# Optimization experiments

Measured on AMD Instinct MI355X. Metric: run time of the kernel, lower is better.

The kernel has to match this reference:

```python
import jax, jax.numpy as jnp
import numpy as np

B, L, H, S2V = 32, 1024, 256, 256
STEP = 1          # HP_SLSTM_step window size
EPS = 1e-3        # LayerNorm eps (added to std, torch-style unbiased std)
NUM_LAYERS = 4
# LayerNorm param row indices in ln_a/ln_b:
# 0..5 -> word gates f1,f2,f3,f4,i,o ; 6 gd ; 7 go ; 8 gf ; 9 gi ; 10 gg


def _ln(x, a, b):
    # torch LayerNorm variant: unbiased std, eps added to std (not var)
    mean = x.mean(-1, keepdims=True)
    d = x - mean
    std = jnp.sqrt((d * d).sum(-1, keepdims=True) / (x.shape[-1] - 1))
    return a * d / (std + EPS) + b


def setup_inputs() -> dict:
    key = jax.random.key(0)
    ks = jax.random.split(key, 16)
    p = lambda k, shp: 0.1 * jax.random.normal(k, shp, dtype=jnp.float32)
    return {
        "word_inputs": jax.random.normal(ks[0], (B, L, H), dtype=jnp.float32),
        "sent_embeddings": jax.random.normal(ks[1], (B, S2V), dtype=jnp.float32),
        "mask": jnp.ones((B, L), dtype=jnp.float32),
        "h0": jax.random.uniform(ks[2], (B, L, H), minval=-0.05, maxval=0.05, dtype=jnp.float32),
        "c0": jax.random.uniform(ks[3], (B, L, H), minval=-0.05, maxval=0.05, dtype=jnp.float32),
        "Wx_g": p(ks[4], (6, H, H)),
        "Wh_g": p(ks[5], (6, 2 * H, H)),
        "Wi_g": p(ks[6], (6, H, H)),
        "Wd_g": p(ks[7], (6, H, H)),
        "b_g": p(ks[8], (6, H)),
        "gWx": p(ks[9], (4, H, H)),   # dummy gates d,i,o,f
        "gWh": p(ks[10], (4, H, H)),
        "gWg": p(ks[11], (4, S2V, H)),  # d,i,o,g
        "gb": p(ks[12], (4, H)),
        "ln_a": jnp.ones((11, H), dtype=jnp.float32),
        "ln_b": jnp.zeros((11, H), dtype=jnp.float32),
        "num_layers": NUM_LAYERS,
    }


def _win_sums(t):
    # sum of left-shifted (before) and right-shifted (after) neighbor states
    bef = jnp.zeros_like(t)
    aft = jnp.zeros_like(t)
    for s in range(1, STEP + 1):
        bef = bef + jnp.pad(t[:, :-s], ((0, 0), (s, 0), (0, 0)))
        aft = aft + jnp.pad(t[:, s:], ((0, 0), (0, s), (0, 0)))
    return bef.reshape(-1, t.shape[-1]), aft.reshape(-1, t.shape[-1])


def reference(word_inputs, sent_embeddings, mask, h0, c0, Wx_g, Wh_g, Wi_g,
              Wd_g, b_g, gWx, gWh, gWg, gb, ln_a, ln_b, num_layers):
    Bs, Ls, Hs = word_inputs.shape
    seq_mask = mask[..., None]                      # (B,L,1)
    msm = (mask * 1e25 - 1e25)[..., None]           # softmax mask (B,L,1)
    emb_h = (word_inputs * seq_mask).reshape(-1, Hs)  # fixed word embedding states
    emb_c = emb_h
    h = h0 * seq_mask
    c = c0 * seq_mask
    dh = h.mean(axis=1)                             # dummy (sentence) node (B,H)
    dc = c.mean(axis=1)

    for _ in range(num_layers):
        comb = h.mean(axis=1)                       # (B,H)
        rh = h.reshape(-1, Hs)                      # (B*L,H)
        tdh = (dh[:, None, :] * seq_mask).reshape(-1, Hs)
        tdc = (dc[:, None, :] * seq_mask).reshape(-1, Hs)

        # --- dummy (sentence-level) node gates ---
        gd = jax.nn.sigmoid(_ln(dh @ gWx[0] + sent_embeddings @ gWg[0] + comb @ gWh[0] + gb[0], ln_a[6], ln_b[6]))
        gi = jax.nn.sigmoid(_ln(dh @ gWx[1] + sent_embeddings @ gWg[1] + comb @ gWh[1], ln_a[9], ln_b[9]) + gb[1])  # bias outside LN, as in source
        gg = sent_embeddings @ gWg[3]
        go = jax.nn.sigmoid(_ln(dh @ gWx[2] + sent_embeddings @ gWg[2] + comb @ gWh[2] + gb[2], ln_a[7], ln_b[7]))
        gf = jax.nn.sigmoid(_ln(tdh @ gWx[3] + rh @ gWh[3] + gb[3], ln_a[8], ln_b[8]))
        gf = gf.reshape(Bs, Ls, Hs) + msm
        scores = jax.nn.softmax(jnp.concatenate([gf, gd[:, None, :], gi[:, None, :]], axis=1), axis=1)
        f_w = scores[:, :Ls]
        d_w = scores[:, Ls]
        i_w = scores[:, Ls + 1]
        dc_new = jnp.sum(f_w * c, axis=1) + d_w * dc + i_w * jnp.tanh(_ln(gg, ln_a[10], ln_b[10]))
        dh_new = go * jnp.tanh(dc_new)

        # --- word node gates (windowed message passing) ---
        hb, ha = _win_sums(h)
        cb, ca = _win_sums(c)
        cat_h = jnp.concatenate([hb, ha], axis=1)   # (B*L, 2H)
        pre = (jnp.einsum('nh,ghk->gnk', emb_h, Wx_g)
               + jnp.einsum('nc,gck->gnk', cat_h, Wh_g)
               + jnp.einsum('nh,ghk->gnk', rh, Wi_g)
               + jnp.einsum('nh,ghk->gnk', tdh, Wd_g)
               + b_g[:, None, :])                   # (6, B*L, H)
        gates = jax.nn.sigmoid(_ln(pre, ln_a[:6, None, :], ln_b[:6, None, :]))
        five = jax.nn.softmax(gates[:5], axis=0)    # normalize f1..f4,i
        f1, f2, f3, f4, i_t = five
        o_t = gates[5]
        c_new = cb * f1 + ca * f2 + emb_c * f3 + tdc * f4 + c.reshape(-1, Hs) * i_t
        h_new = o_t * jnp.tanh(c_new)
        h = h_new.reshape(Bs, Ls, Hs) * seq_mask
        c = c_new.reshape(Bs, Ls, Hs) * seq_mask
        dh, dc = dh_new, dc_new
    return h
```

## Files before the change

kernel.cpp:

```cpp
#include <hip/hip_runtime.h>
#include <cstddef>

#define Bz 32
#define Lz 1024
#define Hz 256
#define Nz (Bz*Lz)
#define NHz ((size_t)Nz*Hz)
#define BHz (Bz*Hz)
#define EPSz 1e-3f
#define NLAYERS 4
#define NCH 64
#define NTC 112
#define CHR 16384

typedef __bf16 bf8_t __attribute__((ext_vector_type(8)));
typedef __bf16 bf4_t __attribute__((ext_vector_type(4)));
typedef float  f4_t  __attribute__((ext_vector_type(4)));

__device__ inline float sigmoidf(float x){ return 1.f/(1.f+expf(-x)); }
__device__ inline float fsig(float x){ return __builtin_amdgcn_rcpf(1.f + __expf(-x)); }
__device__ inline float ftanh(float x){ return 1.f - 2.f*__builtin_amdgcn_rcpf(__expf(2.f*x)+1.f); }

__device__ inline void gl_lds16(const void* g, void* l){
  __builtin_amdgcn_global_load_lds(
      (const __attribute__((address_space(1))) void*)g,
      (__attribute__((address_space(3))) void*)l, 16, 0, 0);
}

__device__ inline float2 block_sum2(float a, float b, float* red){
  #pragma unroll
  for (int off=32; off; off>>=1){ a += __shfl_down(a,off,64); b += __shfl_down(b,off,64); }
  int w = threadIdx.x>>6;
  __syncthreads();
  if ((threadIdx.x&63)==0){ red[w]=a; red[4+w]=b; }
  __syncthreads();
  return make_float2(red[0]+red[1]+red[2]+red[3], red[4]+red[5]+red[6]+red[7]);
}

__device__ inline float ln_block(float v, const float* la, const float* lb, int t, float* red){
  float2 ss = block_sum2(v, v*v, red);
  float mean = ss.x*(1.f/Hz);
  float var  = (ss.y - (float)Hz*mean*mean)*(1.f/(Hz-1));
  float isd  = 1.f/(sqrtf(fmaxf(var,0.f))+EPSz);
  return la[t]*(v-mean)*isd + lb[t];
}

__global__ void k_initb(const float* __restrict__ word, const float* __restrict__ h0,
                        const float* __restrict__ c0, const float* __restrict__ mask,
                        __bf16* __restrict__ xe, __bf16* __restrict__ h, __bf16* __restrict__ c){
  int tid = blockIdx.x*256 + threadIdx.x;
  int n = tid >> 5; int c8 = (tid & 31)*8;
  float m = mask[n];
  size_t off = (size_t)n*Hz + c8;
  const float4* wv = (const float4*)(word + off);
  float4 w0 = wv[0], w1 = wv[1];
  bf8_t o;
  o[0]=(__bf16)(w0.x*m); o[1]=(__bf16)(w0.y*m); o[2]=(__bf16)(w0.z*m); o[3]=(__bf16)(w0.w*m);
  o[4]=(__bf16)(w1.x*m); o[5]=(__bf16)(w1.y*m); o[6]=(__bf16)(w1.z*m); o[7]=(__bf16)(w1.w*m);
  *(bf8_t*)(xe + off) = o;
  const float4* hv = (const float4*)(h0 + off);
  float4 a0 = hv[0], a1 = hv[1];
  o[0]=(__bf16)(a0.x*m); o[1]=(__bf16)(a0.y*m); o[2]=(__bf16)(a0.z*m); o[3]=(__bf16)(a0.w*m);
  o[4]=(__bf16)(a1.x*m); o[5]=(__bf16)(a1.y*m); o[6]=(__bf16)(a1.z*m); o[7]=(__bf16)(a1.w*m);
  *(bf8_t*)(h + off) = o;
  const float4* cv = (const float4*)(c0 + off);
  float4 b0 = cv[0], b1 = cv[1];
  o[0]=(__bf16)(b0.x*m); o[1]=(__bf16)(b0.y*m); o[2]=(__bf16)(b0.z*m); o[3]=(__bf16)(b0.w*m);
  o[4]=(__bf16)(b1.x*m); o[5]=(__bf16)(b1.y*m); o[6]=(__bf16)(b1.z*m); o[7]=(__bf16)(b1.w*m);
  *(bf8_t*)(c + off) = o;
}

__global__ void k_packWt(const float* __restrict__ Wx, const float* __restrict__ Wh,
                         const float* __restrict__ Wi, const float* __restrict__ gWh3,
                         __bf16* __restrict__ Wt, __bf16* __restrict__ zbuf){
  int tid = blockIdx.x*256 + threadIdx.x;
  if (tid < 128) zbuf[tid] = (__bf16)0.f;
  int col = tid >> 7;
  int k0  = (tid & 127) << 3;
  if (col >= 1792) return;
  int g = col >> 8, cg = col & 255;
  int seg = k0 >> 8, kl0 = k0 & 255;
  bf8_t o;
  #pragma unroll
  for (int j=0;j<8;j++){
    int kl = kl0 + j;
    float v = 0.f;
    if (g < 6){
      if (seg==0)      v = Wx[((size_t)g*256 + kl)*256 + cg];
      else if (seg==1) v = Wh[((size_t)g*512 + kl)*256 + cg];
      else if (seg==2) v = Wh[((size_t)g*512 + 256 + kl)*256 + cg];
      else             v = Wi[((size_t)g*256 + kl)*256 + cg];
    } else {
      if (seg==3)      v = gWh3[(size_t)kl*256 + cg];
    }
    o[j] = (__bf16)v;
  }
  *(bf8_t*)(Wt + (size_t)col*1024 + k0) = o;
}

__global__ void k_meanpb(const __bf16* __restrict__ x, float* __restrict__ part){
  int b = blockIdx.x, ch = blockIdx.y, t = threadIdx.x;
  const __bf16* p = x + ((size_t)b*Lz + ch*128)*Hz + t;
  float s = 0.f;
  #pragma unroll 4
  for (int l=0;l<128;l++) s += (float)p[(size_t)l*Hz];
  part[(b*8+ch)*Hz + t] = s;
}
__global__ void k_comb8(const float* __restrict__ part, float* __restrict__ o){
  int b = blockIdx.x, t = threadIdx.x;
  float s = 0.f;
  #pragma unroll
  for (int ch=0;ch<8;ch++) s += part[(b*8+ch)*Hz + t];
  o[b*Hz+t] = s*(1.f/Lz);
}

__global__ __launch_bounds__(256) void k_small(
    const float* __restrict__ dh, const float* __restrict__ comb, const float* __restrict__ sent,
    const float* __restrict__ gWx, const float* __restrict__ gWh, const float* __restrict__ gWg,
    const float* __restrict__ gb, const float* __restrict__ Wd_g,
    const float* __restrict__ ln_a, const float* __restrict__ ln_b,
    float* __restrict__ gd, float* __restrict__ gi, float* __restrict__ go,
    float* __restrict__ tgg, float* __restrict__ dhWd7){
  int b = blockIdx.x, which = blockIdx.y, t = threadIdx.x;
  __shared__ float sdh[Hz], sse[Hz], sco[Hz];
  __shared__ float red[8];
  sdh[t]=dh[b*Hz+t]; sse[t]=sent[b*Hz+t]; sco[t]=comb[b*Hz+t];
  __syncthreads();
  float acc=0.f;
  if (which < 3){
    const float* W0 = gWx + which*Hz*Hz;
    const float* W1 = gWg + which*Hz*Hz;
    const float* W2 = gWh + which*Hz*Hz;
    for (int k=0;k<Hz;k++) acc += sdh[k]*W0[k*Hz+t] + sse[k]*W1[k*Hz+t] + sco[k]*W2[k*Hz+t];
    if (which==0){
      float r = ln_block(acc + gb[0*Hz+t], ln_a+6*Hz, ln_b+6*Hz, t, red);
      gd[b*Hz+t] = sigmoidf(r);
    } else if (which==1){
      float r = ln_block(acc, ln_a+9*Hz, ln_b+9*Hz, t, red);
      gi[b*Hz+t] = sigmoidf(r + gb[1*Hz+t]);
    } else {
      float r = ln_block(acc + gb[2*Hz+t], ln_a+7*Hz, ln_b+7*Hz, t, red);
      go[b*Hz+t] = sigmoidf(r);
    }
  } else if (which == 3){
    const float* W = gWg + 3*Hz*Hz;
    for (int k=0;k<Hz;k++) acc += sse[k]*W[k*Hz+t];
    float r = ln_block(acc, ln_a+10*Hz, ln_b+10*Hz, t, red);
    tgg[b*Hz+t] = tanhf(r);
  } else if (which == 4){
    const float* W = gWx + 3*Hz*Hz;
    for (int k=0;k<Hz;k++) acc += sdh[k]*W[k*Hz+t];
    dhWd7[(6*Bz + b)*Hz + t] = acc;
  } else {
    int g = which-5;
    const float* W = Wd_g + g*Hz*Hz;
    for (int k=0;k<Hz;k++) acc += sdh[k]*W[k*Hz+t];
    dhWd7[(g*Bz + b)*Hz + t] = acc;
  }
}

__global__ __launch_bounds__(256) void k_gemm(
    const __bf16* __restrict__ xe, const __bf16* __restrict__ h,
    const __bf16* __restrict__ Wt, const __bf16* __restrict__ zbuf,
    __bf16* __restrict__ pre, int n_base){
  __shared__ __align__(16) __bf16 sA[128*64];
  __shared__ __align__(16) __bf16 sB[128*64];
  int t = threadIdx.x;
  int w = t>>6, lane = t&63;
  int m16 = lane&15, p = lane>>4;
  int bx = blockIdx.x, by = blockIdx.y;
  int row0 = n_base + bx*128;
  int coltile = by*128;

  f4_t acc[4][4];
  #pragma unroll
  for (int i=0;i<4;i++)
    #pragma unroll
    for (int j=0;j<4;j++) acc[i][j] = (f4_t){0.f,0.f,0.f,0.f};

  int srr = t>>3;
  int sck = t&7;
  int arow = (w&1)*64 + m16;
  int brow = (w>>1)*64 + m16;
  int swz  = m16 & 7;

  const char* Ab = (const char*)sA;
  const char* Bb = (const char*)sB;

  int seg_s = (by >= 12) ? 3 : 0;
  #pragma unroll 1
  for (int seg=seg_s; seg<4; ++seg){
    #pragma unroll 1
    for (int ks=0; ks<4; ++ks){
      __syncthreads();
      int kloc = ks*64;
      #pragma unroll
      for (int it=0; it<4; ++it){
        int drow = it*32 + srr;
        int sc = (sck ^ (drow&7)) << 3;
        int r = row0 + drow;
        const __bf16* asrc;
        if (seg==0)      asrc = xe + (size_t)r*Hz + kloc + sc;
        else if (seg==3) asrc = h + (size_t)r*Hz + kloc + sc;
        else if (seg==1) asrc = ((r&1023)==0)    ? zbuf : h + ((size_t)(r-1)*Hz + kloc + sc);
        else             asrc = ((r&1023)==1023) ? zbuf : h + ((size_t)(r+1)*Hz + kloc + sc);
        gl_lds16(asrc, sA + drow*64 + sck*8);
        const __bf16* bsrc = Wt + (size_t)(coltile + drow)*1024 + seg*256 + kloc + sc;
        gl_lds16(bsrc, sB + drow*64 + sck*8);
      }
      __syncthreads();
      #pragma unroll
      for (int kb=0; kb<2; ++kb){
        bf8_t a[4], bb[4];
        int cofs = ((kb*4 + p) ^ swz) << 4;
        #pragma unroll
        for (int tr=0;tr<4;tr++)
          a[tr] = *(const bf8_t*)(Ab + (arow + tr*16)*128 + cofs);
        #pragma unroll
        for (int tc=0;tc<4;tc++)
          bb[tc] = *(const bf8_t*)(Bb + (brow + tc*16)*128 + cofs);
        #pragma unroll
        for (int tr=0;tr<4;tr++)
          #pragma unroll
          for (int tc=0;tc<4;tc++)
            acc[tr][tc] = __builtin_amdgcn_mfma_f32_16x16x32_bf16(a[tr], bb[tc], acc[tr][tc], 0, 0, 0);
      }
    }
  }

  int trg0 = (bx*128 + (w&1)*64) >> 4;
  int tcg0 = (coltile + (w>>1)*64) >> 4;
  #pragma unroll
  for (int tr=0;tr<4;tr++){
    #pragma unroll
    for (int tc=0;tc<4;tc++){
      size_t tile = (size_t)(trg0+tr)*NTC + (tcg0+tc);
      bf4_t o;
      o[0]=(__bf16)acc[tr][tc][0]; o[1]=(__bf16)acc[tr][tc][1];
      o[2]=(__bf16)acc[tr][tc][2]; o[3]=(__bf16)acc[tr][tc][3];
      *(bf4_t*)(pre + tile*256 + lane*4) = o;
    }
  }
}

__global__ __launch_bounds__(1024) void k_epi(
    const __bf16* __restrict__ pre, const __bf16* __restrict__ xe,
    const __bf16* __restrict__ cc, const float* __restrict__ mask,
    const float* __restrict__ dhWd7, const float* __restrict__ b_g,
    const float* __restrict__ gb3, const float* __restrict__ ln_a, const float* __restrict__ ln_b,
    const float* __restrict__ dc,
    float* __restrict__ outf, __bf16* __restrict__ hn, __bf16* __restrict__ cn,
    float* __restrict__ pm, float* __restrict__ ps, float* __restrict__ pn,
    int n_base, int last){
  __shared__ float sred_s[16][7][16];
  __shared__ float sred_q[16][7][16];
  __shared__ float smean[7][16];
  __shared__ float sisd[7][16];
  __shared__ float hsh[16*260];
  int t = threadIdx.x;
  int n0 = n_base + blockIdx.x*16;
  int b = n0 >> 10;
  int w16 = t>>6, lane = t&63, m16 = lane&15, p = lane>>4;
  int col = w16*16 + m16;
  size_t trk = blockIdx.x;

  bf4_t pv[7];
  float wd[7], bg[7], la[7], lb[7];
  #pragma unroll
  for (int g=0; g<7; ++g){
    size_t tile = trk*NTC + g*16 + w16;
    pv[g] = *(const bf4_t*)(pre + tile*256 + lane*4);
    wd[g] = dhWd7[(g*Bz + b)*Hz + col];
    bg[g] = (g<6) ? b_g[g*Hz + col] : gb3[col];
    int lnr = (g<6) ? g : 8;
    la[g] = ln_a[lnr*Hz+col]; lb[g] = ln_b[lnr*Hz+col];
  }
  float msk4[4], cvv[4], cb4[4], ca4[4], em4[4];
  #pragma unroll
  for (int reg=0; reg<4; ++reg){
    int n2 = n0 + p*4 + reg;
    int l2 = n2 & 1023;
    msk4[reg] = mask[n2];
    cvv[reg] = (float)cc[(size_t)n2*Hz + col];
    cb4[reg] = (l2==0)    ? 0.f : (float)cc[(size_t)(n2-1)*Hz + col];
    ca4[reg] = (l2==1023) ? 0.f : (float)cc[(size_t)(n2+1)*Hz + col];
    em4[reg] = (float)xe[(size_t)n2*Hz + col];
  }
  float tdc = dc[b*Hz + col];

  float acc[7][4];
  #pragma unroll
  for (int g=0; g<7; ++g){
    float s_r[4], q_r[4];
    #pragma unroll
    for (int reg=0; reg<4; ++reg){
      float x = (float)pv[g][reg] + msk4[reg]*wd[g] + bg[g];
      acc[g][reg] = x;
      s_r[reg] = x; q_r[reg] = x*x;
    }
    #pragma unroll
    for (int off=1; off<16; off<<=1){
      #pragma unroll
      for (int reg=0; reg<4; ++reg){
        s_r[reg] += __shfl_xor(s_r[reg], off, 64);
        q_r[reg] += __shfl_xor(q_r[reg], off, 64);
      }
    }
    if (m16==0){
      #pragma unroll
      for (int reg=0; reg<4; ++reg){
        sred_s[w16][g][p*4+reg] = s_r[reg];
        sred_q[w16][g][p*4+reg] = q_r[reg];
      }
    }
  }
  __syncthreads();

  if (t < 112){
    int g = t>>4, row = t&15;
    float ss=0.f, qq=0.f;
    #pragma unroll
    for (int ww=0; ww<16; ++ww){
      ss += sred_s[ww][g][row];
      qq += sred_q[ww][g][row];
    }
    float mean = ss*(1.f/Hz);
    float var  = (qq - (float)Hz*mean*mean)*(1.f/(Hz-1));
    smean[g][row] = mean;
    sisd[g][row]  = __builtin_amdgcn_rcpf(sqrtf(fmaxf(var,0.f))+EPSz);
  }
  __syncthreads();

  #pragma unroll
  for (int g=0; g<7; ++g){
    #pragma unroll
    for (int reg=0; reg<4; ++reg){
      int row = p*4+reg;
      acc[g][reg] = fsig(la[g]*(acc[g][reg]-smean[g][row])*sisd[g][row] + lb[g]);
    }
  }

  {
    float mm = -1e30f, gfv[4];
    #pragma unroll
    for (int reg=0; reg<4; ++reg){
      float gv = acc[6][reg] + (msk4[reg]*1e25f - 1e25f);
      gfv[reg] = gv;
      mm = fmaxf(mm, gv);
    }
    float ss=0.f, nn=0.f;
    #pragma unroll
    for (int reg=0; reg<4; ++reg){
      float e = __expf(gfv[reg]-mm);
      ss += e; nn += e*cvv[reg];
    }
    #pragma unroll
    for (int off=16; off<64; off<<=1){
      float mo = __shfl_xor(mm, off, 64);
      float so = __shfl_xor(ss, off, 64);
      float no = __shfl_xor(nn, off, 64);
      float mN = fmaxf(mm, mo);
      float ea = __expf(mm-mN), eb = __expf(mo-mN);
      ss = ss*ea + so*eb; nn = nn*ea + no*eb; mm = mN;
    }
    if (p==0){
      int ch = (n0 >> 4) & (NCH-1);
      int idx = (b*NCH + ch)*Hz + col;
      pm[idx]=mm; ps[idx]=ss; pn[idx]=nn;
    }
  }

  float cnv[4];
  #pragma unroll
  for (int reg=0; reg<4; ++reg){
    float msk = msk4[reg];
    float g0=acc[0][reg], g1=acc[1][reg], g2=acc[2][reg], g3=acc[3][reg], g4=acc[4][reg];
    float m5 = fmaxf(fmaxf(fmaxf(g0,g1),fmaxf(g2,g3)),g4);
    float e0=__expf(g0-m5), e1=__expf(g1-m5), e2=__expf(g2-m5), e3=__expf(g3-m5), e4=__expf(g4-m5);
    float inv = __builtin_amdgcn_rcpf(e0+e1+e2+e3+e4);
    float cnew = (cb4[reg]*e0 + ca4[reg]*e1 + em4[reg]*e2 + (tdc*msk)*e3 + cvv[reg]*e4)*inv;
    float hv = acc[5][reg]*ftanh(cnew);
    hsh[(p*4+reg)*260 + col] = hv*msk;
    cnv[reg] = cnew*msk;
  }
  __syncthreads();
  {
    int row = t>>6, c4 = lane*4;
    int n = n0 + row;
    const float* src = hsh + row*260 + c4;
    float v0=src[0], v1=src[1], v2=src[2], v3=src[3];
    if (last){
      *(float4*)(outf + (size_t)n*Hz + c4) = make_float4(v0,v1,v2,v3);
    } else {
      bf4_t o; o[0]=(__bf16)v0; o[1]=(__bf16)v1; o[2]=(__bf16)v2; o[3]=(__bf16)v3;
      *(bf4_t*)(hn + (size_t)n*Hz + c4) = o;
    }
  }
  __syncthreads();
  #pragma unroll
  for (int reg=0; reg<4; ++reg) hsh[(p*4+reg)*260 + col] = cnv[reg];
  __syncthreads();
  {
    int row = t>>6, c4 = lane*4;
    const float* src = hsh + row*260 + c4;
    bf4_t o; o[0]=(__bf16)src[0]; o[1]=(__bf16)src[1]; o[2]=(__bf16)src[2]; o[3]=(__bf16)src[3];
    *(bf4_t*)(cn + (size_t)(n0+row)*Hz + c4) = o;
  }
}

__global__ void k_soft_comb(const float* __restrict__ pm, const float* __restrict__ ps,
    const float* __restrict__ pn,
    const float* __restrict__ gd, const float* __restrict__ gi, const float* __restrict__ go,
    const float* __restrict__ tgg, const float* __restrict__ dc,
    float* __restrict__ dc_new, float* __restrict__ dh_new){
  int b = blockIdx.x, t = threadIdx.x;
  float vgd = gd[b*Hz+t], vgi = gi[b*Hz+t];
  float m = fmaxf(vgd, vgi);
  for (int ch=0; ch<NCH; ch++) m = fmaxf(m, pm[(b*NCH+ch)*Hz + t]);
  float ed = expf(vgd - m), ei = expf(vgi - m);
  float s  = ed + ei;
  float num = ed*dc[b*Hz+t] + ei*tgg[b*Hz+t];
  for (int ch=0; ch<NCH; ch++){
    int idx = (b*NCH+ch)*Hz + t;
    float e = expf(pm[idx] - m);
    s   += ps[idx]*e;
    num += pn[idx]*e;
  }
  float dcn = num/s;
  dc_new[b*Hz+t] = dcn;
  dh_new[b*Hz+t] = go[b*Hz+t]*tanhf(dcn);
}

extern "C" void kernel_launch(void* const* d_in, const int* in_sizes, int n_in,
                              void* d_out, int out_size, void* d_ws, size_t ws_size,
                              hipStream_t stream) {
  const float* word  = (const float*)d_in[0];
  const float* sent  = (const float*)d_in[1];
  const float* mask  = (const float*)d_in[2];
  const float* h0    = (const float*)d_in[3];
  const float* c0    = (const float*)d_in[4];
  const float* Wx_g  = (const float*)d_in[5];
  const float* Wh_g  = (const float*)d_in[6];
  const float* Wi_g  = (const float*)d_in[7];
  const float* Wd_g  = (const float*)d_in[8];
  const float* b_g   = (const float*)d_in[9];
  const float* gWx   = (const float*)d_in[10];
  const float* gWh   = (const float*)d_in[11];
  const float* gWg   = (const float*)d_in[12];
  const float* gb    = (const float*)d_in[13];
  const float* ln_a  = (const float*)d_in[14];
  const float* ln_b  = (const float*)d_in[15];
  float* out = (float*)d_out;

  char* wc = (char*)d_ws;
  __bf16* xe  = (__bf16*)wc;  wc += NHz*2;
  __bf16* h_a = (__bf16*)wc;  wc += NHz*2;
  __bf16* h_b = (__bf16*)wc;  wc += NHz*2;
  __bf16* c_a = (__bf16*)wc;  wc += NHz*2;
  __bf16* c_b = (__bf16*)wc;  wc += NHz*2;
  __bf16* pre = (__bf16*)wc;  wc += (size_t)(CHR/16)*NTC*256*2;
  __bf16* Wt  = (__bf16*)wc;  wc += (size_t)1792*1024*2;
  __bf16* zbuf = (__bf16*)wc; wc += 256;
  float* dh_a = (float*)wc;   wc += BHz*4;
  float* dh_b = (float*)wc;   wc += BHz*4;
  float* dc_a = (float*)wc;   wc += BHz*4;
  float* dc_b = (float*)wc;   wc += BHz*4;
  float* comb = (float*)wc;   wc += BHz*4;
  float* gd   = (float*)wc;   wc += BHz*4;
  float* gi_  = (float*)wc;   wc += BHz*4;
  float* go_  = (float*)wc;   wc += BHz*4;
  float* tgg  = (float*)wc;   wc += BHz*4;
  float* dhWd7 = (float*)wc;  wc += 7*BHz*4;
  float* pmean = (float*)wc;  wc += 8*BHz*4;
  float* pm = (float*)wc;     wc += (size_t)Bz*NCH*Hz*4;
  float* ps = (float*)wc;     wc += (size_t)Bz*NCH*Hz*4;
  float* pn = (float*)wc;     wc += (size_t)Bz*NCH*Hz*4;

  k_packWt<<<896, 256, 0, stream>>>(Wx_g, Wh_g, Wi_g, gWh + 3*Hz*Hz, Wt, zbuf);
  k_initb<<<4096, 256, 0, stream>>>(word, h0, c0, mask, xe, h_a, c_a);
  k_meanpb<<<dim3(Bz,8), 256, 0, stream>>>(h_a, pmean);
  k_comb8<<<Bz, 256, 0, stream>>>(pmean, dh_a);
  k_meanpb<<<dim3(Bz,8), 256, 0, stream>>>(c_a, pmean);
  k_comb8<<<Bz, 256, 0, stream>>>(pmean, dc_a);

  __bf16* hc=h_a; __bf16* hn=h_b;
  __bf16* cc=c_a; __bf16* cn=c_b;
  float* dhc=dh_a; float* dcc=dc_a; float* dhn=dh_b; float* dcn=dc_b;

  for (int layer=0; layer<NLAYERS; ++layer){
    k_meanpb<<<dim3(Bz,8), 256, 0, stream>>>(hc, pmean);
    k_comb8<<<Bz, 256, 0, stream>>>(pmean, comb);
    k_small<<<dim3(Bz,11), 256, 0, stream>>>(dhc, comb, sent, gWx, gWh, gWg, gb, Wd_g,
                                             ln_a, ln_b, gd, gi_, go_, tgg, dhWd7);
    int last = (layer == NLAYERS-1) ? 1 : 0;
    for (int chunk=0; chunk<Nz/CHR; ++chunk){
      int n_base = chunk*CHR;
      k_gemm<<<dim3(CHR/128, 14), 256, 0, stream>>>(xe, hc, Wt, zbuf, pre, n_base);
      k_epi<<<CHR/16, 1024, 0, stream>>>(pre, xe, cc, mask, dhWd7, b_g, gb + 3*Hz,
                                         ln_a, ln_b, dcc, out, hn, cn, pm, ps, pn,
                                         n_base, last);
    }
    k_soft_comb<<<Bz, 256, 0, stream>>>(pm, ps, pn, gd, gi_, go_, tgg, dcc, dcn, dhn);
    __bf16* tb;
    tb=hc; hc=hn; hn=tb;
    tb=cc; cc=cn; cn=tb;
    float* tmp;
    tmp=dhc; dhc=dhn; dhn=tmp;
    tmp=dcc; dcc=dcn; dcn=tmp;
  }
  (void)in_sizes; (void)n_in; (void)out_size; (void)ws_size;
}
```

Measured before the change: 1.460 ms.

## Double-buffer GEMM LDS tiles and use DPP row reductions in epilogue

```diff
diff --git a/kernel.cpp b/kernel.cpp
--- a/kernel.cpp
+++ b/kernel.cpp
@@ -20,6 +20,19 @@
 __device__ inline float sigmoidf(float x){ return 1.f/(1.f+expf(-x)); }
 __device__ inline float fsig(float x){ return __builtin_amdgcn_rcpf(1.f + __expf(-x)); }
 __device__ inline float ftanh(float x){ return 1.f - 2.f*__builtin_amdgcn_rcpf(__expf(2.f*x)+1.f); }
+
+template<int C>
+__device__ inline float dppadd(float v){
+  int t = __builtin_amdgcn_update_dpp(0, __builtin_bit_cast(int, v), C, 0xf, 0xf, true);
+  return v + __builtin_bit_cast(float, t);
+}
+__device__ inline float dppsum16(float v){
+  v = dppadd<0x111>(v);
+  v = dppadd<0x112>(v);
+  v = dppadd<0x114>(v);
+  v = dppadd<0x118>(v);
+  return v;
+}
 
 __device__ inline void gl_lds16(const void* g, void* l){
   __builtin_amdgcn_global_load_lds(
@@ -163,8 +176,8 @@
     const __bf16* __restrict__ xe, const __bf16* __restrict__ h,
     const __bf16* __restrict__ Wt, const __bf16* __restrict__ zbuf,
     __bf16* __restrict__ pre, int n_base){
-  __shared__ __align__(16) __bf16 sA[128*64];
-  __shared__ __align__(16) __bf16 sB[128*64];
+  __shared__ __align__(16) __bf16 sA[2][128*64];
+  __shared__ __align__(16) __bf16 sB[2][128*64];
   int t = threadIdx.x;
   int w = t>>6, lane = t&63;
   int m16 = lane&15, p = lane>>4;
@@ -184,48 +197,52 @@
   int brow = (w>>1)*64 + m16;
   int swz  = m16 & 7;
 
-  const char* Ab = (const char*)sA;
-  const char* Bb = (const char*)sB;
-
-  int seg_s = (by >= 12) ? 3 : 0;
+  auto STAGE = [&](int kk, int buf){
+    int seg = kk>>2;
+    int kloc = (kk&3)*64;
+    #pragma unroll
+    for (int it=0; it<4; ++it){
+      int drow = it*32 + srr;
+      int sc = (sck ^ (drow&7)) << 3;
+      int r = row0 + drow;
+      const __bf16* asrc;
+      if (seg==0)      asrc = xe + (size_t)r*Hz + kloc + sc;
+      else if (seg==3) asrc = h + (size_t)r*Hz + kloc + sc;
+      else if (seg==1) asrc = ((r&1023)==0)    ? zbuf : h + ((size_t)(r-1)*Hz + kloc + sc);
+      else             asrc = ((r&1023)==1023) ? zbuf : h + ((size_t)(r+1)*Hz + kloc + sc);
+      gl_lds16(asrc, &sA[buf][drow*64 + sck*8]);
+      const __bf16* bsrc = Wt + (size_t)(coltile + drow)*1024 + seg*256 + kloc + sc;
+      gl_lds16(bsrc, &sB[buf][drow*64 + sck*8]);
+    }
+  };
+
+  int kk_s = (by >= 12) ? 12 : 0;
+  STAGE(kk_s, 0);
+  __syncthreads();
+  int cur = 0;
   #pragma unroll 1
-  for (int seg=seg_s; seg<4; ++seg){
-    #pragma unroll 1
-    for (int ks=0; ks<4; ++ks){
-      __syncthreads();
-      int kloc = ks*64;
+  for (int kk=kk_s; kk<16; ++kk){
+    if (kk < 15) STAGE(kk+1, cur^1);
+    const char* Ab = (const char*)sA[cur];
+    const char* Bb = (const char*)sB[cur];
+    #pragma unroll
+    for (int kb=0; kb<2; ++kb){
+      bf8_t a[4], bb[4];
+      int cofs = ((kb*4 + p) ^ swz) << 4;
       #pragma unroll
-      for (int it=0; it<4; ++it){
-        int drow = it*32 + srr;
-        int sc = (sck ^ (drow&7)) << 3;
-        int r = row0 + drow;
-        const __bf16* asrc;
-        if (seg==0)      asrc = xe + (size_t)r*Hz + kloc + sc;
-        else if (seg==3) asrc = h + (size_t)r*Hz + kloc + sc;
-        else if (seg==1) asrc = ((r&1023)==0)    ? zbuf : h + ((size_t)(r-1)*Hz + kloc + sc);
-        else             asrc = ((r&1023)==1023) ? zbuf : h + ((size_t)(r+1)*Hz + kloc + sc);
-        gl_lds16(asrc, sA + drow*64 + sck*8);
-        const __bf16* bsrc = Wt + (size_t)(coltile + drow)*1024 + seg*256 + kloc + sc;
-        gl_lds16(bsrc, sB + drow*64 + sck*8);
-      }
-      __syncthreads();
+      for (int tr=0;tr<4;tr++)
+        a[tr] = *(const bf8_t*)(Ab + (arow + tr*16)*128 + cofs);
       #pragma unroll
-      for (int kb=0; kb<2; ++kb){
-        bf8_t a[4], bb[4];
-        int cofs = ((kb*4 + p) ^ swz) << 4;
-        #pragma unroll
-        for (int tr=0;tr<4;tr++)
-          a[tr] = *(const bf8_t*)(Ab + (arow + tr*16)*128 + cofs);
+      for (int tc=0;tc<4;tc++)
+        bb[tc] = *(const bf8_t*)(Bb + (brow + tc*16)*128 + cofs);
+      #pragma unroll
+      for (int tr=0;tr<4;tr++)
         #pragma unroll
         for (int tc=0;tc<4;tc++)
-          bb[tc] = *(const bf8_t*)(Bb + (brow + tc*16)*128 + cofs);
-        #pragma unroll
-        for (int tr=0;tr<4;tr++)
-          #pragma unroll
-          for (int tc=0;tc<4;tc++)
-            acc[tr][tc] = __builtin_amdgcn_mfma_f32_16x16x32_bf16(a[tr], bb[tc], acc[tr][tc], 0, 0, 0);
-      }
-    }
+          acc[tr][tc] = __builtin_amdgcn_mfma_f32_16x16x32_bf16(a[tr], bb[tc], acc[tr][tc], 0, 0, 0);
+    }
+    __syncthreads();
+    cur ^= 1;
   }
 
   int trg0 = (bx*128 + (w&1)*64) >> 4;
@@ -296,17 +313,10 @@
     for (int reg=0; reg<4; ++reg){
       float x = (float)pv[g][reg] + msk4[reg]*wd[g] + bg[g];
       acc[g][reg] = x;
-      s_r[reg] = x; q_r[reg] = x*x;
-    }
-    #pragma unroll
-    for (int off=1; off<16; off<<=1){
-      #pragma unroll
-      for (int reg=0; reg<4; ++reg){
-        s_r[reg] += __shfl_xor(s_r[reg], off, 64);
-        q_r[reg] += __shfl_xor(q_r[reg], off, 64);
-      }
-    }
-    if (m16==0){
+      s_r[reg] = dppsum16(x);
+      q_r[reg] = dppsum16(x*x);
+    }
+    if (m16==15){
       #pragma unroll
       for (int reg=0; reg<4; ++reg){
         sred_s[w16][g][p*4+reg] = s_r[reg];
```

Result: faster. 1.383 ms, median of 2 (-5.3%).
